# Kernel optimization log

Hardware: AMD Instinct MI355X
Metric: run time of the kernel (lower is better)

The kernel has to match this reference:

```python
import jax, jax.numpy as jnp
import numpy as np

INPUT_SIZE = 512
HIDDEN = 1024

def setup_inputs() -> dict:
    key = jax.random.key(0)
    k1, k2, k3, k4, k5 = jax.random.split(key, 5)
    sx = 1.0 / np.sqrt(INPUT_SIZE)
    sh = 1.0 / np.sqrt(HIDDEN)
    return {
        "x": jax.random.normal(k1, (32, 512, INPUT_SIZE), dtype=jnp.float32),
        "Wx": jax.random.uniform(k2, (4 * HIDDEN, INPUT_SIZE), jnp.float32, -sx, sx),
        "bx": jax.random.uniform(k3, (4 * HIDDEN,), jnp.float32, -sx, sx),
        "Wh": jax.random.uniform(k4, (4 * HIDDEN, HIDDEN), jnp.float32, -sh, sh),
        "bh": jax.random.uniform(k5, (4 * HIDDEN,), jnp.float32, -sh, sh),
    }

def reference(x, Wx, bx, Wh, bh):
    B, T, _ = x.shape
    H = Wh.shape[1]
    # Precompute input projections for all timesteps in one GEMM: [B,T,4H]
    xg = jnp.einsum('bti,gi->btg', x, Wx) + bx + bh
    h0 = jnp.zeros((B, H), x.dtype)
    c0 = jnp.zeros((B, H), x.dtype)

    def step(carry, xg_t):
        h, c = carry
        gates = xg_t + h @ Wh.T  # [B,4H]
        i, f, g, o = jnp.split(gates, 4, axis=1)
        i = jax.nn.sigmoid(i)
        f = jax.nn.sigmoid(f)
        g = jnp.tanh(g)
        o = jax.nn.sigmoid(o)
        c = c * f + i * g
        h = o * jnp.tanh(c)
        return (h, c), h

    _, hs = jax.lax.scan(step, (h0, c0), jnp.swapaxes(xg, 0, 1))  # hs: [T,B,H]
    return jnp.swapaxes(hs, 0, 1)  # [B,T,H]
```

## Files before the change

kernel.cpp:

```cpp
#include <hip/hip_runtime.h>
#include <hip/hip_bf16.h>

typedef _Float16 f16x8 __attribute__((ext_vector_type(8)));
typedef float f32x4 __attribute__((ext_vector_type(4)));
typedef unsigned int u32;
typedef unsigned long long u64;

constexpr int kIN = 512;
constexpr int kHID = 1024;
constexpr int kGH = 4096;
constexpr int kT = 512;
constexpr int kB = 32;

constexpr size_t OFF_XG   = 0;
constexpr size_t OFF_XH   = 134217728;
constexpr size_t OFF_WXH  = 150994944;
constexpr size_t OFF_WHH  = 155189248;
constexpr size_t OFF_BIAS = 163577856;
constexpr size_t OFF_HBUF = 163594240;
constexpr size_t OFF_CNT  = 163725312;
constexpr size_t WS_NEED  = 163856384;

__device__ __forceinline__ float sigm_f(float x) {
  x = fminf(fmaxf(x, -30.f), 30.f);
  return 1.f / (1.f + __expf(-x));
}
__device__ __forceinline__ float tanh_f(float x) {
  x = fminf(fmaxf(x, -15.f), 15.f);
  float e = __expf(2.f * x);
  return (e - 1.f) / (e + 1.f);
}

__global__ void k0_prep(const float* __restrict__ x, const float* __restrict__ Wx,
                        const float* __restrict__ bx, const float* __restrict__ Wh,
                        const float* __restrict__ bh,
                        _Float16* __restrict__ xh, _Float16* __restrict__ wxh,
                        _Float16* __restrict__ whh, float* __restrict__ bias,
                        u32* __restrict__ cnt) {
  const long NX = 8388608, NWX = 2097152, NWH = 4194304, NBI = 4096, NFL = 8192;
  const long total = NX + NWX + NWH + NBI + NFL;
  for (long i = (long)blockIdx.x * blockDim.x + threadIdx.x; i < total;
       i += (long)gridDim.x * blockDim.x) {
    long j = i;
    if (j < NX) { xh[j] = (_Float16)x[j]; continue; }
    j -= NX;
    if (j < NWX) { wxh[j] = (_Float16)Wx[j]; continue; }
    j -= NWX;
    if (j < NWH) { whh[j] = (_Float16)Wh[j]; continue; }
    j -= NWH;
    if (j < NBI) { bias[j] = bx[j] + bh[j]; continue; }
    j -= NBI;
    __hip_atomic_store(&cnt[j], 0u, __ATOMIC_RELAXED, __HIP_MEMORY_SCOPE_AGENT);
  }
}

__global__ __launch_bounds__(256) void k1_xgemm(const _Float16* __restrict__ A,
                                                const _Float16* __restrict__ Bm,
                                                const float* __restrict__ bias,
                                                _Float16* __restrict__ C) {
  __shared__ _Float16 sA[128 * 32];
  __shared__ _Float16 sB[128 * 32];
  const int tid = threadIdx.x;
  const int lane = tid & 63, w = tid >> 6;
  const long m0 = (long)blockIdx.x * 128;
  const long n0 = (long)blockIdx.y * 128;
  const int wm = (w & 1) * 64, wn = (w >> 1) * 64;
  const int fr = lane & 15, fk = (lane >> 4) * 8;

  f32x4 acc[4][4] = {};

  for (int k0 = 0; k0 < kIN; k0 += 32) {
#pragma unroll
    for (int it = 0; it < 2; ++it) {
      int c = it * 256 + tid;
      int row = c >> 2, seg = c & 3;
      *(f16x8*)&sA[c * 8] = *(const f16x8*)&A[(m0 + row) * kIN + k0 + seg * 8];
      *(f16x8*)&sB[c * 8] = *(const f16x8*)&Bm[(n0 + row) * kIN + k0 + seg * 8];
    }
    __syncthreads();
    f16x8 af[4], bf[4];
#pragma unroll
    for (int t = 0; t < 4; ++t) {
      af[t] = *(const f16x8*)&sA[(wm + t * 16 + fr) * 32 + fk];
      bf[t] = *(const f16x8*)&sB[(wn + t * 16 + fr) * 32 + fk];
    }
#pragma unroll
    for (int mt = 0; mt < 4; ++mt)
#pragma unroll
      for (int nt = 0; nt < 4; ++nt)
        acc[mt][nt] = __builtin_amdgcn_mfma_f32_16x16x32_f16(af[mt], bf[nt], acc[mt][nt], 0, 0, 0);
    __syncthreads();
  }

  const int cn = lane & 15, cm4 = (lane >> 4) * 4;
#pragma unroll
  for (int nt = 0; nt < 4; ++nt) {
    long col = n0 + wn + nt * 16 + cn;
    float bv = bias[col];
#pragma unroll
    for (int mt = 0; mt < 4; ++mt)
#pragma unroll
      for (int r = 0; r < 4; ++r) {
        long row = m0 + wm + mt * 16 + cm4 + r;
        C[row * kGH + col] = (_Float16)(acc[mt][nt][r] + bv);
      }
  }
}

__global__ __launch_bounds__(256, 1) void k2_rec(const _Float16* __restrict__ xg,
                                                 const _Float16* __restrict__ whh,
                                                 u32* __restrict__ hbuf,
                                                 u32* __restrict__ cnt,
                                                 float* __restrict__ out) {
  const int tid = threadIdx.x;
  const int lane = tid & 63, w = tid >> 6;
  const int bid = blockIdx.x;
  const int jb = bid * 16;

  __shared__ float part[4 * 64 * 35];

  const int fr = lane & 15;
  const int fq = lane >> 4;

  f16x8 bfr[4][8];
#pragma unroll
  for (int nt = 0; nt < 4; ++nt) {
    long grow = (long)(nt * kHID + jb + fr) * kHID;
#pragma unroll
    for (int kt = 0; kt < 8; ++kt)
      bfr[nt][kt] = *(const f16x8*)&whh[grow + w * 256 + kt * 32 + fq * 8];
  }

  const int eb = tid >> 3;
  const int jp = tid & 7;
  float cst0 = 0.f, cst1 = 0.f;
  bool last = false;

  for (int t = 0; t < kT; ++t) {
    u32 xv[4];
    {
      const u32* xgu = (const u32*)xg;
      long rowbase = ((long)eb * kT + t) * (kGH / 2) + bid * 8 + jp;
#pragma unroll
      for (int g = 0; g < 4; ++g) xv[g] = xgu[rowbase + g * (kHID / 2)];
    }

    if (t > 0) {
      if (w == 0 && !last) {
        const u32* cp = &cnt[(size_t)(t - 1) * 16];
        while (__hip_atomic_load(cp, __ATOMIC_RELAXED, __HIP_MEMORY_SCOPE_AGENT) < 64u) {
        }
      }
    }
    __syncthreads();

    f32x4 acc[2][4] = {};
    if (t > 0) {
      const u64* hp64 = (const u64*)(hbuf + ((t & 1) ^ 1) * (kB * kHID / 2));
      u64 hr[2][8][2];
#pragma unroll
      for (int kt = 0; kt < 8; ++kt) {
        int cidx = w * 64 + kt * 8 + fq * 2;
#pragma unroll
        for (int q = 0; q < 2; ++q) {
          hr[0][kt][q] = __hip_atomic_load(&hp64[(size_t)fr * 256 + cidx + q],
                                           __ATOMIC_RELAXED, __HIP_MEMORY_SCOPE_AGENT);
          hr[1][kt][q] = __hip_atomic_load(&hp64[(size_t)(fr + 16) * 256 + cidx + q],
                                           __ATOMIC_RELAXED, __HIP_MEMORY_SCOPE_AGENT);
        }
      }
#pragma unroll
      for (int kt = 0; kt < 8; ++kt) {
        union { u64 u[2]; f16x8 v; } ua, ub;
        ua.u[0] = hr[0][kt][0]; ua.u[1] = hr[0][kt][1];
        ub.u[0] = hr[1][kt][0]; ub.u[1] = hr[1][kt][1];
#pragma unroll
        for (int nt = 0; nt < 4; ++nt) {
          acc[0][nt] = __builtin_amdgcn_mfma_f32_16x16x32_f16(ua.v, bfr[nt][kt], acc[0][nt], 0, 0, 0);
          acc[1][nt] = __builtin_amdgcn_mfma_f32_16x16x32_f16(ub.v, bfr[nt][kt], acc[1][nt], 0, 0, 0);
        }
      }
    }

#pragma unroll
    for (int mt = 0; mt < 2; ++mt)
#pragma unroll
      for (int nt = 0; nt < 4; ++nt)
        *(f32x4*)&part[(w * 64 + nt * 16 + fr) * 35 + mt * 16 + fq * 4] = acc[mt][nt];
    __syncthreads();

    float g0[4], g1[4];
#pragma unroll
    for (int g = 0; g < 4; ++g) {
      union { u32 u; _Float16 h[2]; } xu;
      xu.u = xv[g];
      float s0 = (float)xu.h[0], s1 = (float)xu.h[1];
      int n0 = g * 16 + jp * 2;
#pragma unroll
      for (int wv = 0; wv < 4; ++wv) {
        s0 += part[(wv * 64 + n0) * 35 + eb];
        s1 += part[(wv * 64 + n0 + 1) * 35 + eb];
      }
      g0[g] = s0; g1[g] = s1;
    }
    float h0, h1;
    {
      float ig = sigm_f(g0[0]), fg = sigm_f(g0[1]);
      float gg = tanh_f(g0[2]), og = sigm_f(g0[3]);
      cst0 = cst0 * fg + ig * gg;
      h0 = og * tanh_f(cst0);
    }
    {
      float ig = sigm_f(g1[0]), fg = sigm_f(g1[1]);
      float gg = tanh_f(g1[2]), og = sigm_f(g1[3]);
      cst1 = cst1 * fg + ig * gg;
      h1 = og * tanh_f(cst1);
    }

    union { u32 u; _Float16 h[2]; } pk;
    pk.h[0] = (_Float16)h0; pk.h[1] = (_Float16)h1;
    __hip_atomic_store(&hbuf[(t & 1) * (kB * kHID / 2) + eb * (kHID / 2) + bid * 8 + jp],
                       pk.u, __ATOMIC_RELAXED, __HIP_MEMORY_SCOPE_AGENT);

    __syncthreads();

    u32 old = 0;
    if (tid == 0)
      old = __hip_atomic_fetch_add(&cnt[(size_t)t * 16], 1u, __ATOMIC_RELEASE,
                                   __HIP_MEMORY_SCOPE_AGENT);
    last = (__builtin_amdgcn_readfirstlane(old) == 63u);

    *(float2*)&out[((long)eb * kT + t) * kHID + jb + jp * 2] = make_float2(h0, h1);
  }
}

extern "C" void kernel_launch(void* const* d_in, const int* in_sizes, int n_in,
                              void* d_out, int out_size, void* d_ws, size_t ws_size,
                              hipStream_t stream) {
  const float* x  = (const float*)d_in[0];
  const float* Wx = (const float*)d_in[1];
  const float* bx = (const float*)d_in[2];
  const float* Wh = (const float*)d_in[3];
  const float* bh = (const float*)d_in[4];
  float* out = (float*)d_out;

  if (ws_size < WS_NEED) return;

  char* ws = (char*)d_ws;
  _Float16* xg    = (_Float16*)(ws + OFF_XG);
  _Float16* xh    = (_Float16*)(ws + OFF_XH);
  _Float16* wxh   = (_Float16*)(ws + OFF_WXH);
  _Float16* whh   = (_Float16*)(ws + OFF_WHH);
  float*    bias  = (float*)(ws + OFF_BIAS);
  u32*      hbuf  = (u32*)(ws + OFF_HBUF);
  u32*      cnt   = (u32*)(ws + OFF_CNT);

  hipLaunchKernelGGL(k0_prep, dim3(4096), dim3(256), 0, stream,
                     x, Wx, bx, Wh, bh, xh, wxh, whh, bias, cnt);
  hipLaunchKernelGGL(k1_xgemm, dim3(128, 32), dim3(256), 0, stream,
                     xh, wxh, bias, xg);
  hipLaunchKernelGGL(k2_rec, dim3(64), dim3(256), 0, stream,
                     xg, whh, hbuf, cnt, out);
}
```

Before: 4.289 ms.

## Replace counter barrier with sentinel-flagged 4-slot h ring buffer

Removes the per-step global atomic counter barrier between the 64 recurrent blocks. Each hidden-state word in a 4-slot ring now acts as its own readiness flag: a slot is reset to a sentinel two steps ahead, and readers spin until no loaded value equals the sentinel. This drops the fetch_add, the single-wave spin and one block barrier per step, letting each block start as soon as its data arrives. It relies on a half-precision h pair never matching the sentinel bit pattern and on the relaxed ordering of the reset store against the later data store.

Result: faster. 3.923 ms (-8.5%).

```diff
diff --git a/kernel.cpp b/kernel.cpp
--- a/kernel.cpp
+++ b/kernel.cpp
@@ -12,14 +12,15 @@
 constexpr int kT = 512;
 constexpr int kB = 32;
 
-constexpr size_t OFF_XG   = 0;
-constexpr size_t OFF_XH   = 134217728;
-constexpr size_t OFF_WXH  = 150994944;
-constexpr size_t OFF_WHH  = 155189248;
-constexpr size_t OFF_BIAS = 163577856;
-constexpr size_t OFF_HBUF = 163594240;
-constexpr size_t OFF_CNT  = 163725312;
-constexpr size_t WS_NEED  = 163856384;
+constexpr u32 SENT32 = 0x7FFF7FFFu;
+
+constexpr size_t OFF_XG    = 0;
+constexpr size_t OFF_XH    = 134217728;
+constexpr size_t OFF_WXH   = 150994944;
+constexpr size_t OFF_WHH   = 155189248;
+constexpr size_t OFF_BIAS  = 163577856;
+constexpr size_t OFF_HRING = 163594240;
+constexpr size_t WS_NEED   = 163856384;
 
 __device__ __forceinline__ float sigm_f(float x) {
   x = fminf(fmaxf(x, -30.f), 30.f);
@@ -36,9 +37,9 @@
                         const float* __restrict__ bh,
                         _Float16* __restrict__ xh, _Float16* __restrict__ wxh,
                         _Float16* __restrict__ whh, float* __restrict__ bias,
-                        u32* __restrict__ cnt) {
-  const long NX = 8388608, NWX = 2097152, NWH = 4194304, NBI = 4096, NFL = 8192;
-  const long total = NX + NWX + NWH + NBI + NFL;
+                        u32* __restrict__ hring) {
+  const long NX = 8388608, NWX = 2097152, NWH = 4194304, NBI = 4096, NRG = 65536;
+  const long total = NX + NWX + NWH + NBI + NRG;
   for (long i = (long)blockIdx.x * blockDim.x + threadIdx.x; i < total;
        i += (long)gridDim.x * blockDim.x) {
     long j = i;
@@ -50,7 +51,7 @@
     j -= NWH;
     if (j < NBI) { bias[j] = bx[j] + bh[j]; continue; }
     j -= NBI;
-    __hip_atomic_store(&cnt[j], 0u, __ATOMIC_RELAXED, __HIP_MEMORY_SCOPE_AGENT);
+    __hip_atomic_store(&hring[j], SENT32, __ATOMIC_RELAXED, __HIP_MEMORY_SCOPE_AGENT);
   }
 }
 
@@ -109,8 +110,7 @@
 
 __global__ __launch_bounds__(256, 1) void k2_rec(const _Float16* __restrict__ xg,
                                                  const _Float16* __restrict__ whh,
-                                                 u32* __restrict__ hbuf,
-                                                 u32* __restrict__ cnt,
+                                                 u32* __restrict__ hring,
                                                  float* __restrict__ out) {
   const int tid = threadIdx.x;
   const int lane = tid & 63, w = tid >> 6;
@@ -134,9 +134,13 @@
   const int eb = tid >> 3;
   const int jp = tid & 7;
   float cst0 = 0.f, cst1 = 0.f;
-  bool last = false;
 
   for (int t = 0; t < kT; ++t) {
+    const int wslot = t & 3, rslot = (t - 1) & 3, zslot = (t + 1) & 3;
+
+    __hip_atomic_store(&hring[zslot * 16384 + eb * 512 + bid * 8 + jp], SENT32,
+                       __ATOMIC_RELAXED, __HIP_MEMORY_SCOPE_AGENT);
+
     u32 xv[4];
     {
       const u32* xgu = (const u32*)xg;
@@ -145,29 +149,35 @@
       for (int g = 0; g < 4; ++g) xv[g] = xgu[rowbase + g * (kHID / 2)];
     }
 
-    if (t > 0) {
-      if (w == 0 && !last) {
-        const u32* cp = &cnt[(size_t)(t - 1) * 16];
-        while (__hip_atomic_load(cp, __ATOMIC_RELAXED, __HIP_MEMORY_SCOPE_AGENT) < 64u) {
-        }
-      }
-    }
-    __syncthreads();
-
     f32x4 acc[2][4] = {};
     if (t > 0) {
-      const u64* hp64 = (const u64*)(hbuf + ((t & 1) ^ 1) * (kB * kHID / 2));
+      const u64* hp64 = (const u64*)(hring + rslot * 16384);
       u64 hr[2][8][2];
-#pragma unroll
-      for (int kt = 0; kt < 8; ++kt) {
-        int cidx = w * 64 + kt * 8 + fq * 2;
-#pragma unroll
-        for (int q = 0; q < 2; ++q) {
-          hr[0][kt][q] = __hip_atomic_load(&hp64[(size_t)fr * 256 + cidx + q],
-                                           __ATOMIC_RELAXED, __HIP_MEMORY_SCOPE_AGENT);
-          hr[1][kt][q] = __hip_atomic_load(&hp64[(size_t)(fr + 16) * 256 + cidx + q],
-                                           __ATOMIC_RELAXED, __HIP_MEMORY_SCOPE_AGENT);
+      while (true) {
+#pragma unroll
+        for (int kt = 0; kt < 8; ++kt) {
+          int cidx = w * 64 + kt * 8 + fq * 2;
+#pragma unroll
+          for (int q = 0; q < 2; ++q) {
+            hr[0][kt][q] = __hip_atomic_load(&hp64[(size_t)fr * 256 + cidx + q],
+                                             __ATOMIC_RELAXED, __HIP_MEMORY_SCOPE_AGENT);
+            hr[1][kt][q] = __hip_atomic_load(&hp64[(size_t)(fr + 16) * 256 + cidx + q],
+                                             __ATOMIC_RELAXED, __HIP_MEMORY_SCOPE_AGENT);
+          }
         }
+        u32 bad = 0;
+#pragma unroll
+        for (int m = 0; m < 2; ++m)
+#pragma unroll
+          for (int kt = 0; kt < 8; ++kt)
+#pragma unroll
+            for (int q = 0; q < 2; ++q) {
+              u64 v = hr[m][kt][q];
+              bad |= ((u32)v == SENT32) | ((u32)(v >> 32) == SENT32);
+            }
+        if (!__any(bad)) break;
+        __builtin_amdgcn_s_sleep(1);
+        asm volatile("" ::: "memory");
       }
 #pragma unroll
       for (int kt = 0; kt < 8; ++kt) {
@@ -203,6 +213,8 @@
       }
       g0[g] = s0; g1[g] = s1;
     }
+    __syncthreads();
+
     float h0, h1;
     {
       float ig = sigm_f(g0[0]), fg = sigm_f(g0[1]);
@@ -217,18 +229,12 @@
       h1 = og * tanh_f(cst1);
     }
 
+    asm volatile("s_waitcnt vmcnt(0)" ::: "memory");
+
     union { u32 u; _Float16 h[2]; } pk;
     pk.h[0] = (_Float16)h0; pk.h[1] = (_Float16)h1;
-    __hip_atomic_store(&hbuf[(t & 1) * (kB * kHID / 2) + eb * (kHID / 2) + bid * 8 + jp],
+    __hip_atomic_store(&hring[wslot * 16384 + eb * 512 + bid * 8 + jp],
                        pk.u, __ATOMIC_RELAXED, __HIP_MEMORY_SCOPE_AGENT);
-
-    __syncthreads();
-
-    u32 old = 0;
-    if (tid == 0)
-      old = __hip_atomic_fetch_add(&cnt[(size_t)t * 16], 1u, __ATOMIC_RELEASE,
-                                   __HIP_MEMORY_SCOPE_AGENT);
-    last = (__builtin_amdgcn_readfirstlane(old) == 63u);
 
     *(float2*)&out[((long)eb * kT + t) * kHID + jb + jp * 2] = make_float2(h0, h1);
   }
@@ -252,13 +258,12 @@
   _Float16* wxh   = (_Float16*)(ws + OFF_WXH);
   _Float16* whh   = (_Float16*)(ws + OFF_WHH);
   float*    bias  = (float*)(ws + OFF_BIAS);
-  u32*      hbuf  = (u32*)(ws + OFF_HBUF);
-  u32*      cnt   = (u32*)(ws + OFF_CNT);
+  u32*      hring = (u32*)(ws + OFF_HRING);
 
   hipLaunchKernelGGL(k0_prep, dim3(4096), dim3(256), 0, stream,
-                     x, Wx, bx, Wh, bh, xh, wxh, whh, bias, cnt);
+                     x, Wx, bx, Wh, bh, xh, wxh, whh, bias, hring);
   hipLaunchKernelGGL(k1_xgemm, dim3(128, 32), dim3(256), 0, stream,
                      xh, wxh, bias, xg);
   hipLaunchKernelGGL(k2_rec, dim3(64), dim3(256), 0, stream,
-                     xg, whh, hbuf, cnt, out);
-}
+                     xg, whh, hring, out);
+}
```

## Replace atomic counter barrier with per-block flags and prefetch blocked xg

Applied to the files above, without the earlier changes.

The per-step grid barrier changes from one atomic counter that all 64 blocks fetch-add into a per-timestep array of 64 flags. Each block writes its own flag and wave 0 polls all flags in parallel with a wave-wide __all. The xgemm output is re-laid out as [t][block][gate][batch][16] so each block's slice for a step is contiguous, and the next step's slice is prefetched into registers before the recurrence needs it. h is now read with plain vector loads after an acquire fence rather than relaxed atomics, which removes contention on the counter but makes the flag array 4x larger.

After: 4.031 ms. 6.0% less time.

```diff
diff --git a/kernel.cpp b/kernel.cpp
--- a/kernel.cpp
+++ b/kernel.cpp
@@ -12,14 +12,14 @@
 constexpr int kT = 512;
 constexpr int kB = 32;
 
-constexpr size_t OFF_XG   = 0;
-constexpr size_t OFF_XH   = 134217728;
-constexpr size_t OFF_WXH  = 150994944;
-constexpr size_t OFF_WHH  = 155189248;
-constexpr size_t OFF_BIAS = 163577856;
-constexpr size_t OFF_HBUF = 163594240;
-constexpr size_t OFF_CNT  = 163725312;
-constexpr size_t WS_NEED  = 163856384;
+constexpr size_t OFF_XG    = 0;
+constexpr size_t OFF_XH    = 134217728;
+constexpr size_t OFF_WXH   = 150994944;
+constexpr size_t OFF_WHH   = 155189248;
+constexpr size_t OFF_BIAS  = 163577856;
+constexpr size_t OFF_HBUF  = 163594240;
+constexpr size_t OFF_FLAG  = 163725312;
+constexpr size_t WS_NEED   = 163856384;
 
 __device__ __forceinline__ float sigm_f(float x) {
   x = fminf(fmaxf(x, -30.f), 30.f);
@@ -36,8 +36,8 @@
                         const float* __restrict__ bh,
                         _Float16* __restrict__ xh, _Float16* __restrict__ wxh,
                         _Float16* __restrict__ whh, float* __restrict__ bias,
-                        u32* __restrict__ cnt) {
-  const long NX = 8388608, NWX = 2097152, NWH = 4194304, NBI = 4096, NFL = 8192;
+                        u32* __restrict__ flags) {
+  const long NX = 8388608, NWX = 2097152, NWH = 4194304, NBI = 4096, NFL = 32768;
   const long total = NX + NWX + NWH + NBI + NFL;
   for (long i = (long)blockIdx.x * blockDim.x + threadIdx.x; i < total;
        i += (long)gridDim.x * blockDim.x) {
@@ -50,7 +50,7 @@
     j -= NWH;
     if (j < NBI) { bias[j] = bx[j] + bh[j]; continue; }
     j -= NBI;
-    __hip_atomic_store(&cnt[j], 0u, __ATOMIC_RELAXED, __HIP_MEMORY_SCOPE_AGENT);
+    __hip_atomic_store(&flags[j], 0u, __ATOMIC_RELAXED, __HIP_MEMORY_SCOPE_AGENT);
   }
 }
 
@@ -97,12 +97,14 @@
   for (int nt = 0; nt < 4; ++nt) {
     long col = n0 + wn + nt * 16 + cn;
     float bv = bias[col];
+    long g = col >> 10, bx = (col >> 4) & 63, jj = col & 15;
 #pragma unroll
     for (int mt = 0; mt < 4; ++mt)
 #pragma unroll
       for (int r = 0; r < 4; ++r) {
         long row = m0 + wm + mt * 16 + cm4 + r;
-        C[row * kGH + col] = (_Float16)(acc[mt][nt][r] + bv);
+        long b = row >> 9, tt = row & 511;
+        C[(((tt * 64 + bx) * 4 + g) * 32 + b) * 16 + jj] = (_Float16)(acc[mt][nt][r] + bv);
       }
   }
 }
@@ -110,7 +112,7 @@
 __global__ __launch_bounds__(256, 1) void k2_rec(const _Float16* __restrict__ xg,
                                                  const _Float16* __restrict__ whh,
                                                  u32* __restrict__ hbuf,
-                                                 u32* __restrict__ cnt,
+                                                 u32* __restrict__ flags,
                                                  float* __restrict__ out) {
   const int tid = threadIdx.x;
   const int lane = tid & 63, w = tid >> 6;
@@ -134,50 +136,49 @@
   const int eb = tid >> 3;
   const int jp = tid & 7;
   float cst0 = 0.f, cst1 = 0.f;
-  bool last = false;
+
+  const u32* xgu = (const u32*)xg;
+  u32 xn[4];
+#pragma unroll
+  for (int g = 0; g < 4; ++g)
+    xn[g] = xgu[(size_t)((0 * 64 + bid) * 4 + g) * 256 + eb * 8 + jp];
 
   for (int t = 0; t < kT; ++t) {
+    if (t > 0) {
+      if (w == 0) {
+        const u32* fl = flags + (size_t)(t - 1) * 64;
+        while (true) {
+          u32 f = (lane == bid)
+                      ? 1u
+                      : __hip_atomic_load(&fl[lane], __ATOMIC_RELAXED,
+                                          __HIP_MEMORY_SCOPE_AGENT);
+          if (__all(f != 0)) break;
+        }
+      }
+      __syncthreads();
+      __builtin_amdgcn_fence(__ATOMIC_ACQUIRE, "agent");
+    }
+
     u32 xv[4];
-    {
-      const u32* xgu = (const u32*)xg;
-      long rowbase = ((long)eb * kT + t) * (kGH / 2) + bid * 8 + jp;
-#pragma unroll
-      for (int g = 0; g < 4; ++g) xv[g] = xgu[rowbase + g * (kHID / 2)];
-    }
-
-    if (t > 0) {
-      if (w == 0 && !last) {
-        const u32* cp = &cnt[(size_t)(t - 1) * 16];
-        while (__hip_atomic_load(cp, __ATOMIC_RELAXED, __HIP_MEMORY_SCOPE_AGENT) < 64u) {
-        }
-      }
-    }
-    __syncthreads();
+#pragma unroll
+    for (int g = 0; g < 4; ++g) xv[g] = xn[g];
+    if (t + 1 < kT) {
+#pragma unroll
+      for (int g = 0; g < 4; ++g)
+        xn[g] = xgu[(size_t)(((t + 1) * 64 + bid) * 4 + g) * 256 + eb * 8 + jp];
+    }
 
     f32x4 acc[2][4] = {};
     if (t > 0) {
-      const u64* hp64 = (const u64*)(hbuf + ((t & 1) ^ 1) * (kB * kHID / 2));
-      u64 hr[2][8][2];
+      const _Float16* hb = (const _Float16*)(hbuf + ((t & 1) ^ 1) * 16384);
 #pragma unroll
       for (int kt = 0; kt < 8; ++kt) {
-        int cidx = w * 64 + kt * 8 + fq * 2;
-#pragma unroll
-        for (int q = 0; q < 2; ++q) {
-          hr[0][kt][q] = __hip_atomic_load(&hp64[(size_t)fr * 256 + cidx + q],
-                                           __ATOMIC_RELAXED, __HIP_MEMORY_SCOPE_AGENT);
-          hr[1][kt][q] = __hip_atomic_load(&hp64[(size_t)(fr + 16) * 256 + cidx + q],
-                                           __ATOMIC_RELAXED, __HIP_MEMORY_SCOPE_AGENT);
-        }
-      }
-#pragma unroll
-      for (int kt = 0; kt < 8; ++kt) {
-        union { u64 u[2]; f16x8 v; } ua, ub;
-        ua.u[0] = hr[0][kt][0]; ua.u[1] = hr[0][kt][1];
-        ub.u[0] = hr[1][kt][0]; ub.u[1] = hr[1][kt][1];
+        f16x8 a0 = *(const f16x8*)&hb[(size_t)fr * 1024 + w * 256 + kt * 32 + fq * 8];
+        f16x8 a1 = *(const f16x8*)&hb[(size_t)(fr + 16) * 1024 + w * 256 + kt * 32 + fq * 8];
 #pragma unroll
         for (int nt = 0; nt < 4; ++nt) {
-          acc[0][nt] = __builtin_amdgcn_mfma_f32_16x16x32_f16(ua.v, bfr[nt][kt], acc[0][nt], 0, 0, 0);
-          acc[1][nt] = __builtin_amdgcn_mfma_f32_16x16x32_f16(ub.v, bfr[nt][kt], acc[1][nt], 0, 0, 0);
+          acc[0][nt] = __builtin_amdgcn_mfma_f32_16x16x32_f16(a0, bfr[nt][kt], acc[0][nt], 0, 0, 0);
+          acc[1][nt] = __builtin_amdgcn_mfma_f32_16x16x32_f16(a1, bfr[nt][kt], acc[1][nt], 0, 0, 0);
         }
       }
     }
@@ -203,6 +204,7 @@
       }
       g0[g] = s0; g1[g] = s1;
     }
+
     float h0, h1;
     {
       float ig = sigm_f(g0[0]), fg = sigm_f(g0[1]);
@@ -219,16 +221,15 @@
 
     union { u32 u; _Float16 h[2]; } pk;
     pk.h[0] = (_Float16)h0; pk.h[1] = (_Float16)h1;
-    __hip_atomic_store(&hbuf[(t & 1) * (kB * kHID / 2) + eb * (kHID / 2) + bid * 8 + jp],
+    __hip_atomic_store(&hbuf[(t & 1) * 16384 + eb * 512 + bid * 8 + jp],
                        pk.u, __ATOMIC_RELAXED, __HIP_MEMORY_SCOPE_AGENT);
 
-    __syncthreads();
-
-    u32 old = 0;
+    asm volatile("s_waitcnt vmcnt(0)" ::: "memory");
+    __syncthreads();
+
     if (tid == 0)
-      old = __hip_atomic_fetch_add(&cnt[(size_t)t * 16], 1u, __ATOMIC_RELEASE,
-                                   __HIP_MEMORY_SCOPE_AGENT);
-    last = (__builtin_amdgcn_readfirstlane(old) == 63u);
+      __hip_atomic_store(&flags[(size_t)t * 64 + bid], 1u, __ATOMIC_RELAXED,
+                         __HIP_MEMORY_SCOPE_AGENT);
 
     *(float2*)&out[((long)eb * kT + t) * kHID + jb + jp * 2] = make_float2(h0, h1);
   }
@@ -253,12 +254,12 @@
   _Float16* whh   = (_Float16*)(ws + OFF_WHH);
   float*    bias  = (float*)(ws + OFF_BIAS);
   u32*      hbuf  = (u32*)(ws + OFF_HBUF);
-  u32*      cnt   = (u32*)(ws + OFF_CNT);
+  u32*      flags = (u32*)(ws + OFF_FLAG);
 
   hipLaunchKernelGGL(k0_prep, dim3(4096), dim3(256), 0, stream,
-                     x, Wx, bx, Wh, bh, xh, wxh, whh, bias, cnt);
+                     x, Wx, bx, Wh, bh, xh, wxh, whh, bias, flags);
   hipLaunchKernelGGL(k1_xgemm, dim3(128, 32), dim3(256), 0, stream,
                      xh, wxh, bias, xg);
   hipLaunchKernelGGL(k2_rec, dim3(64), dim3(256), 0, stream,
-                     xg, whh, hbuf, cnt, out);
-}
+                     xg, whh, hbuf, flags, out);
+}
```
